# Kernel tuning notes

Hardware: AMD Instinct MI355X
Metric: run time of the kernel (lower is better)

## Reference

```python
import jax, jax.numpy as jnp
import numpy as np

NUM_EMBED = 1024
HEAD_SIZE = 64
B, T = 4, 4096

def setup_inputs() -> dict:
    key = jax.random.key(0)
    kx, kq, kk, kv = jax.random.split(key, 4)
    scale = NUM_EMBED ** -0.5
    return {
        "x": jax.random.normal(kx, (B, T, NUM_EMBED), dtype=jnp.float32),
        "Wq": jax.random.normal(kq, (NUM_EMBED, HEAD_SIZE), dtype=jnp.float32) * scale,
        "Wk": jax.random.normal(kk, (NUM_EMBED, HEAD_SIZE), dtype=jnp.float32) * scale,
        "Wv": jax.random.normal(kv, (NUM_EMBED, HEAD_SIZE), dtype=jnp.float32) * scale,
    }

def reference(x, Wq, Wk, Wv):
    # x: [B,T,C]; Wq/Wk/Wv: [C,H]
    q = jnp.einsum('btc,ch->bth', x, Wq)
    k = jnp.einsum('btc,ch->bth', x, Wk)
    v = jnp.einsum('btc,ch->bth', x, Wv)
    Tq = x.shape[1]
    att = jnp.einsum('bth,bsh->bts', q, k) * (k.shape[-1] ** -0.5)  # [B,T,T]
    causal = jnp.tril(jnp.ones((Tq, Tq), dtype=bool))
    att = jnp.where(causal, att, -jnp.inf)
    att = jax.nn.softmax(att, axis=-1)
    # dropout p=0 (eval mode): identity
    out = jnp.einsum('bts,bsh->bth', att, v)  # [B,T,H]
    return out
```

## Files before the change

### kernel.cpp

```cpp
#include <hip/hip_runtime.h>

#define B_ 4
#define T_ 4096
#define C_ 1024
#define H_ 64

typedef _Float16 half8  __attribute__((ext_vector_type(8)));
typedef _Float16 half4_ __attribute__((ext_vector_type(4)));
typedef float    floatx4 __attribute__((ext_vector_type(4)));

#define MFMA16(a, b, c)  __builtin_amdgcn_mfma_f32_16x16x32_f16(a, b, c, 0, 0, 0)
#define MFMA16K(a, b, c) __builtin_amdgcn_mfma_f32_16x16x16f16(a, b, c, 0, 0, 0)
#define LO4(v) __builtin_shufflevector(v, v, 0, 1, 2, 3)
#define HI4(v) __builtin_shufflevector(v, v, 4, 5, 6, 7)

__global__ __launch_bounds__(256) void pack_w_kn(
    const float* __restrict__ Wq, const float* __restrict__ Wk,
    const float* __restrict__ Wv, _Float16* __restrict__ Wt2)
{
    const int idx  = blockIdx.x * 256 + threadIdx.x;
    const int mt   = idx >> 14;
    const int j    = (idx >> 10) & 15;
    const int f    = (idx >> 9) & 1;
    const int lane = (idx >> 3) & 63;
    const int jj   = idx & 7;
    const int q = lane >> 4, c = lane & 15;
    const int k  = j * 64 + f * 32 + q * 8 + jj;
    const int hp = mt * 16 + c;
    const float* W = (hp < 64) ? Wq : (hp < 128) ? Wk : Wv;
    Wt2[idx] = (_Float16)W[k * H_ + (hp & 63)];
}

__global__ __launch_bounds__(512) void qkv_kn(
    const float* __restrict__ x, const _Float16* __restrict__ Wt2,
    _Float16* __restrict__ Qh, _Float16* __restrict__ Kpk,
    _Float16* __restrict__ Vpk)
{
    __shared__ _Float16 xs[2][32][72];
    const int tid  = threadIdx.x;
    const int lane = tid & 63, w = tid >> 6;
    const int q    = lane >> 4, c = lane & 15;
    const int nt   = w & 1;
    const int mg   = w >> 1;
    const int row0 = blockIdx.x * 32;

    const int srow = tid >> 4, scol = (tid & 15) * 4;
    const float* xg = x + (size_t)(row0 + srow) * C_ + scol;

    floatx4 acc[3];
    #pragma unroll
    for (int i = 0; i < 3; ++i) acc[i] = floatx4{0.f, 0.f, 0.f, 0.f};

    float4 g = *(const float4*)xg;

    for (int j = 0; j < 16; ++j) {
        half4_ hv;
        hv[0] = (_Float16)g.x; hv[1] = (_Float16)g.y;
        hv[2] = (_Float16)g.z; hv[3] = (_Float16)g.w;
        *(half4_*)(&xs[j & 1][srow][scol]) = hv;
        __syncthreads();
        if (j < 15) g = *(const float4*)(xg + (j + 1) * 64);

        const _Float16* xrow = &xs[j & 1][nt * 16 + c][q * 8];
        const half8 b0 = *(const half8*)xrow;
        const half8 b1 = *(const half8*)(xrow + 32);

        half8 a[6];
        #pragma unroll
        for (int i = 0; i < 3; ++i) {
            const size_t fb = ((size_t)((mg * 3 + i) * 16 + j) * 2) * 512 + lane * 8;
            a[i * 2]     = *(const half8*)(Wt2 + fb);
            a[i * 2 + 1] = *(const half8*)(Wt2 + fb + 512);
        }
        #pragma unroll
        for (int i = 0; i < 3; ++i) {
            acc[i] = MFMA16(a[i * 2],     b0, acc[i]);
            acc[i] = MFMA16(a[i * 2 + 1], b1, acc[i]);
        }
    }

    const int row = row0 + nt * 16 + c;
    const int b = row >> 12, t4 = row & (T_ - 1);
    const int kt = t4 >> 6;
    const size_t tbase = ((size_t)b * 64 + kt) * 4096;
    const int mtk = (t4 >> 4) & 3;
    const int kk  = t4 & 63;

    #pragma unroll
    for (int i = 0; i < 3; ++i) {
        const int gi = mg * 3 + i;
        if (gi < 4) {
            half4_ v;
            #pragma unroll
            for (int r = 0; r < 4; ++r) v[r] = (_Float16)acc[i][r];
            *(half4_*)(Qh + (size_t)row * H_ + gi * 16 + q * 4) = v;
        } else if (gi < 8) {
            half4_ v;
            #pragma unroll
            for (int r = 0; r < 4; ++r) v[r] = (_Float16)acc[i][r];
            const int e  = gi - 4;
            const int f  = e >> 1;
            const int qa = (e * 2 + (q >> 1)) & 3;
            *(half4_*)(Kpk + tbase + ((size_t)(mtk * 2 + f) * 64 + qa * 16 + c) * 8
                       + (q & 1) * 4) = v;
        } else {
            const int mtv = gi - 8;
            const int qa2 = (kk >> 2) & 3;
            const int h4  = (kk >> 4) & 1;
            const int f2  = kk >> 5;
            const int i2  = kk & 3;
            #pragma unroll
            for (int r = 0; r < 4; ++r) {
                const int cv = q * 4 + r;
                Vpk[tbase + ((size_t)(mtv * 2 + f2) * 64 + qa2 * 16 + cv) * 8
                    + h4 * 4 + i2] = (_Float16)acc[i][r];
            }
        }
    }
}

__global__ __launch_bounds__(512, 4) void attn_kn(
    const _Float16* __restrict__ Qh, const _Float16* __restrict__ Kpk,
    const _Float16* __restrict__ Vpk, float* __restrict__ out)
{
    __shared__ __align__(16) char smem[36864];
    const int lane = threadIdx.x & 63;
    const int w    = threadIdx.x >> 6;
    const int q    = lane >> 4, c = lane & 15;

    const int bid  = blockIdx.x;
    const int xcd  = bid & 7;
    const int slot = bid >> 3;
    const int b    = xcd >> 1;
    const int t    = 255 - ((slot << 1) | (xcd & 1));
    const int row0 = t * 16;
    const int grow = b * T_ + row0;
    const int nk   = (t >> 2) + 1;

    half8 bq0 = *(const half8*)(Qh + (size_t)(grow + c) * H_ + q * 8);
    half8 bq1 = *(const half8*)(Qh + (size_t)(grow + c) * H_ + 32 + q * 8);
    const _Float16 qs = (_Float16)0.18033688f;
    bq0 *= qs; bq1 *= qs;

    floatx4 o[4];
    #pragma unroll
    for (int i = 0; i < 4; ++i) o[i] = floatx4{0.f, 0.f, 0.f, 0.f};
    float m = -3.0e38f, l = 0.f;

    const _Float16* Kb = Kpk + (size_t)b * 262144;
    const _Float16* Vb = Vpk + (size_t)b * 262144;

    half8 k0[4], k1[4], v0[4], v1[4];
    {
        const _Float16* Kt = Kb + (size_t)w * 4096;
        #pragma unroll
        for (int mt = 0; mt < 4; ++mt) {
            k0[mt] = *(const half8*)(Kt + ((mt * 2)     * 64 + lane) * 8);
            k1[mt] = *(const half8*)(Kt + ((mt * 2 + 1) * 64 + lane) * 8);
        }
    }

    #pragma unroll 1
    for (int kt = w; kt < nk; kt += 8) {
        const int kb = kt * 64;

        floatx4 s[4];
        __builtin_amdgcn_s_setprio(1);
        #pragma unroll
        for (int mt = 0; mt < 4; ++mt) {
            floatx4 z = floatx4{0.f, 0.f, 0.f, 0.f};
            z = MFMA16(k0[mt], bq0, z);
            s[mt] = MFMA16(k1[mt], bq1, z);
        }
        __builtin_amdgcn_s_setprio(0);

        const _Float16* Vt = Vb + (size_t)kt * 4096;
        #pragma unroll
        for (int mt = 0; mt < 4; ++mt) {
            v0[mt] = *(const half8*)(Vt + ((mt * 2)     * 64 + lane) * 8);
            v1[mt] = *(const half8*)(Vt + ((mt * 2 + 1) * 64 + lane) * 8);
        }
        {
            const int ktn = (kt + 8 < nk) ? (kt + 8) : kt;
            const _Float16* Kt = Kb + (size_t)ktn * 4096;
            #pragma unroll
            for (int mt = 0; mt < 4; ++mt) {
                k0[mt] = *(const half8*)(Kt + ((mt * 2)     * 64 + lane) * 8);
                k1[mt] = *(const half8*)(Kt + ((mt * 2 + 1) * 64 + lane) * 8);
            }
        }

        if (kt == nk - 1) {
            #pragma unroll
            for (int mt = 0; mt < 4; ++mt)
                #pragma unroll
                for (int r = 0; r < 4; ++r)
                    if (kb + mt * 16 + q * 4 + r > row0 + c) s[mt][r] = -3.0e38f;
        }

        float mx = s[0][0];
        #pragma unroll
        for (int mt = 0; mt < 4; ++mt)
            #pragma unroll
            for (int r = 0; r < 4; ++r) mx = fmaxf(mx, s[mt][r]);
        mx = fmaxf(mx, __shfl_xor(mx, 16, 64));
        mx = fmaxf(mx, __shfl_xor(mx, 32, 64));
        if (!__all(mx <= m + 8.f)) {
            const float mn    = fmaxf(m, mx);
            const float alpha = exp2f(m - mn);
            l *= alpha;
            #pragma unroll
            for (int mt = 0; mt < 4; ++mt) o[mt] *= alpha;
            m = mn;
        }
        half4_ ph[4];
        float sl = 0.f;
        #pragma unroll
        for (int mt = 0; mt < 4; ++mt)
            #pragma unroll
            for (int r = 0; r < 4; ++r) {
                const float ev = exp2f(s[mt][r] - m);
                sl += ev;
                ph[mt][r] = (_Float16)ev;
            }
        sl += __shfl_xor(sl, 16, 64);
        sl += __shfl_xor(sl, 32, 64);
        l += sl;

        __builtin_amdgcn_s_setprio(1);
        #pragma unroll
        for (int mt = 0; mt < 4; ++mt) {
            o[mt] = MFMA16K(LO4(v0[mt]), ph[0], o[mt]);
            o[mt] = MFMA16K(HI4(v0[mt]), ph[1], o[mt]);
            o[mt] = MFMA16K(LO4(v1[mt]), ph[2], o[mt]);
            o[mt] = MFMA16K(HI4(v1[mt]), ph[3], o[mt]);
        }
        __builtin_amdgcn_s_setprio(0);
    }

    float* Ol = (float*)smem;
    float* Ml = (float*)(smem + 34816);
    float* Ll = (float*)(smem + 35328);
    if (q == 0) Ml[w * 16 + c] = m;
    __syncthreads();
    float M = Ml[c];
    #pragma unroll
    for (int w2 = 1; w2 < 8; ++w2) M = fmaxf(M, Ml[w2 * 16 + c]);
    const float alpha = exp2f(m - M);
    if (q == 0) Ll[w * 16 + c] = l * alpha;
    #pragma unroll
    for (int mt = 0; mt < 4; ++mt)
        #pragma unroll
        for (int r = 0; r < 4; ++r)
            Ol[w * 1088 + (mt * 16 + q * 4 + r) * 17 + c] = o[mt][r] * alpha;
    __syncthreads();

    float L = 0.f;
    #pragma unroll
    for (int w2 = 0; w2 < 8; ++w2) L += Ll[w2 * 16 + c];
    const float inv = 1.f / L;
    const int h0 = w * 8 + q * 2;
    float ox = 0.f, oy = 0.f;
    #pragma unroll
    for (int w2 = 0; w2 < 8; ++w2) {
        ox += Ol[w2 * 1088 + h0 * 17 + c];
        oy += Ol[w2 * 1088 + (h0 + 1) * 17 + c];
    }
    float2 st; st.x = ox * inv; st.y = oy * inv;
    *(float2*)(out + (size_t)(grow + c) * H_ + h0) = st;
}

extern "C" void kernel_launch(void* const* d_in, const int* in_sizes, int n_in,
                              void* d_out, int out_size, void* d_ws, size_t ws_size,
                              hipStream_t stream) {
    const float* x  = (const float*)d_in[0];
    const float* Wq = (const float*)d_in[1];
    const float* Wk = (const float*)d_in[2];
    const float* Wv = (const float*)d_in[3];
    float* out = (float*)d_out;

    _Float16* ws = (_Float16*)d_ws;
    _Float16* Wt2 = ws;
    _Float16* Qh  = ws + 196608;
    _Float16* Kpk = Qh + 1048576;
    _Float16* Vpk = Kpk + 1048576;

    hipLaunchKernelGGL(pack_w_kn, dim3(768), dim3(256), 0, stream, Wq, Wk, Wv, Wt2);
    hipLaunchKernelGGL(qkv_kn, dim3((B_ * T_) / 32), dim3(512), 0, stream,
                       x, Wt2, Qh, Kpk, Vpk);
    hipLaunchKernelGGL(attn_kn, dim3(1024), dim3(512), 0, stream,
                       Qh, Kpk, Vpk, out);
}
```

Measured before the change: 138.0 us.

## Share K/V tiles across warps via LDS and split-K with separate combine kernel

Each attention block now covers 128 query rows, eight waves of 16 rows each, and one of eight interleaved key-tile slices. K/V tiles are staged into double-buffered shared memory so all eight waves reuse the same loaded tile. Partial outputs, row maxima and row sums are written to workspace, and a new combine kernel merges the eight splits and writes the final output. This cuts redundant global K/V traffic per query row but adds block-wide syncs, a large fp32 partial-output round trip through memory, and an extra kernel launch.

```diff
diff --git a/kernel.cpp b/kernel.cpp
--- a/kernel.cpp
+++ b/kernel.cpp
@@ -121,24 +121,30 @@
 
 __global__ __launch_bounds__(512, 4) void attn_kn(
     const _Float16* __restrict__ Qh, const _Float16* __restrict__ Kpk,
-    const _Float16* __restrict__ Vpk, float* __restrict__ out)
+    const _Float16* __restrict__ Vpk, float* __restrict__ Opart,
+    float* __restrict__ Mp, float* __restrict__ Lp)
 {
-    __shared__ __align__(16) char smem[36864];
-    const int lane = threadIdx.x & 63;
-    const int w    = threadIdx.x >> 6;
+    __shared__ __align__(16) _Float16 KVs[2][2][4096];
+    const int tid  = threadIdx.x;
+    const int lane = tid & 63;
+    const int w    = tid >> 6;
     const int q    = lane >> 4, c = lane & 15;
 
     const int bid  = blockIdx.x;
     const int xcd  = bid & 7;
     const int slot = bid >> 3;
     const int b    = xcd >> 1;
-    const int t    = 255 - ((slot << 1) | (xcd & 1));
-    const int row0 = t * 16;
-    const int grow = b * T_ + row0;
-    const int nk   = (t >> 2) + 1;
-
-    half8 bq0 = *(const half8*)(Qh + (size_t)(grow + c) * H_ + q * 8);
-    half8 bq1 = *(const half8*)(Qh + (size_t)(grow + c) * H_ + 32 + q * 8);
+    const int tau  = 31 - (slot >> 2);
+    const int s    = ((slot & 3) << 1) | (xcd & 1);
+    const int row0 = tau * 128;
+    const int wrow0 = row0 + w * 16;
+    const int nk_blk = 2 * tau + 2;
+    const int nk_w   = (wrow0 >> 6) + 1;
+    const int ntb = (s < nk_blk) ? (((nk_blk - 1 - s) >> 3) + 1) : 0;
+
+    const _Float16* qb = Qh + (size_t)(b * T_ + wrow0 + c) * H_;
+    half8 bq0 = *(const half8*)(qb + q * 8);
+    half8 bq1 = *(const half8*)(qb + 32 + q * 8);
     const _Float16 qs = (_Float16)0.18033688f;
     bq0 *= qs; bq1 *= qs;
 
@@ -150,124 +156,181 @@
     const _Float16* Kb = Kpk + (size_t)b * 262144;
     const _Float16* Vb = Vpk + (size_t)b * 262144;
 
-    half8 k0[4], k1[4], v0[4], v1[4];
-    {
-        const _Float16* Kt = Kb + (size_t)w * 4096;
+    if (ntb > 0) {
+        const _Float16* Kt = Kb + (size_t)s * 4096;
+        const _Float16* Vt = Vb + (size_t)s * 4096;
+        *(half8*)(&KVs[0][0][tid * 8]) = *(const half8*)(Kt + tid * 8);
+        *(half8*)(&KVs[0][1][tid * 8]) = *(const half8*)(Vt + tid * 8);
+    }
+    __syncthreads();
+
+    #pragma unroll 1
+    for (int i = 0; i < ntb; ++i) {
+        const int kt = s + 8 * i;
+        const bool more = (i + 1 < ntb);
+        half8 gk, gv;
+        if (more) {
+            const _Float16* Kt = Kb + (size_t)(kt + 8) * 4096;
+            const _Float16* Vt = Vb + (size_t)(kt + 8) * 4096;
+            gk = *(const half8*)(Kt + tid * 8);
+            gv = *(const half8*)(Vt + tid * 8);
+        }
+
+        if (kt < nk_w) {
+            const _Float16* Ks = &KVs[i & 1][0][0];
+            const _Float16* Vs = &KVs[i & 1][1][0];
+
+            floatx4 sS[4];
+            __builtin_amdgcn_s_setprio(1);
+            #pragma unroll
+            for (int mt = 0; mt < 4; ++mt) {
+                const half8 ka = *(const half8*)(Ks + ((mt * 2)     * 64 + lane) * 8);
+                const half8 kb2= *(const half8*)(Ks + ((mt * 2 + 1) * 64 + lane) * 8);
+                floatx4 z = floatx4{0.f, 0.f, 0.f, 0.f};
+                z = MFMA16(ka, bq0, z);
+                sS[mt] = MFMA16(kb2, bq1, z);
+            }
+            __builtin_amdgcn_s_setprio(0);
+
+            if (kt == nk_w - 1) {
+                const int kb0 = kt * 64;
+                #pragma unroll
+                for (int mt = 0; mt < 4; ++mt)
+                    #pragma unroll
+                    for (int r = 0; r < 4; ++r)
+                        if (kb0 + mt * 16 + q * 4 + r > wrow0 + c)
+                            sS[mt][r] = -3.0e38f;
+            }
+
+            float mx = sS[0][0];
+            #pragma unroll
+            for (int mt = 0; mt < 4; ++mt)
+                #pragma unroll
+                for (int r = 0; r < 4; ++r) mx = fmaxf(mx, sS[mt][r]);
+            mx = fmaxf(mx, __shfl_xor(mx, 16, 64));
+            mx = fmaxf(mx, __shfl_xor(mx, 32, 64));
+            if (!__all(mx <= m + 8.f)) {
+                const float mn    = fmaxf(m, mx);
+                const float alpha = exp2f(m - mn);
+                l *= alpha;
+                #pragma unroll
+                for (int mt = 0; mt < 4; ++mt) o[mt] *= alpha;
+                m = mn;
+            }
+            half4_ ph[4];
+            float sl = 0.f;
+            #pragma unroll
+            for (int mt = 0; mt < 4; ++mt)
+                #pragma unroll
+                for (int r = 0; r < 4; ++r) {
+                    const float ev = exp2f(sS[mt][r] - m);
+                    sl += ev;
+                    ph[mt][r] = (_Float16)ev;
+                }
+            sl += __shfl_xor(sl, 16, 64);
+            sl += __shfl_xor(sl, 32, 64);
+            l += sl;
+
+            __builtin_amdgcn_s_setprio(1);
+            #pragma unroll
+            for (int mt = 0; mt < 4; ++mt) {
+                const half8 va = *(const half8*)(Vs + ((mt * 2)     * 64 + lane) * 8);
+                const half8 vb = *(const half8*)(Vs + ((mt * 2 + 1) * 64 + lane) * 8);
+                o[mt] = MFMA16K(LO4(va), ph[0], o[mt]);
+                o[mt] = MFMA16K(HI4(va), ph[1], o[mt]);
+                o[mt] = MFMA16K(LO4(vb), ph[2], o[mt]);
+                o[mt] = MFMA16K(HI4(vb), ph[3], o[mt]);
+            }
+            __builtin_amdgcn_s_setprio(0);
+        }
+
+        __syncthreads();
+        if (more) {
+            *(half8*)(&KVs[(i + 1) & 1][0][tid * 8]) = gk;
+            *(half8*)(&KVs[(i + 1) & 1][1][tid * 8]) = gv;
+            __syncthreads();
+        }
+    }
+
+    float* Ob = Opart + ((size_t)bid * 8 + w) * 1024;
+    #pragma unroll
+    for (int mt = 0; mt < 4; ++mt)
+        *(floatx4*)(Ob + mt * 256 + lane * 4) = o[mt];
+    if (q == 0) {
+        Mp[(size_t)bid * 128 + w * 16 + c] = m;
+        Lp[(size_t)bid * 128 + w * 16 + c] = l;
+    }
+}
+
+__global__ __launch_bounds__(64) void combine_kn(
+    const float* __restrict__ Opart, const float* __restrict__ Mp,
+    const float* __restrict__ Lp, float* __restrict__ out)
+{
+    __shared__ float sO[64][17];
+    const int cb  = blockIdx.x;
+    const int w2  = cb & 7;
+    const int tau = (cb >> 3) & 31;
+    const int b   = cb >> 8;
+    const int lane = threadIdx.x;
+    const int q = lane >> 4, c = lane & 15;
+
+    int items[8];
+    #pragma unroll
+    for (int s = 0; s < 8; ++s) {
+        const int xcd  = b * 2 + (s & 1);
+        const int slot = (31 - tau) * 4 + (s >> 1);
+        items[s] = slot * 8 + xcd;
+    }
+
+    float Mv[8], Lv[8];
+    #pragma unroll
+    for (int s = 0; s < 8; ++s) {
+        Mv[s] = Mp[(size_t)items[s] * 128 + w2 * 16 + c];
+        Lv[s] = Lp[(size_t)items[s] * 128 + w2 * 16 + c];
+    }
+    float M = Mv[0];
+    #pragma unroll
+    for (int s = 1; s < 8; ++s) M = fmaxf(M, Mv[s]);
+    float L = 0.f;
+    float a[8];
+    #pragma unroll
+    for (int s = 0; s < 8; ++s) {
+        a[s] = exp2f(Mv[s] - M);
+        L += Lv[s] * a[s];
+    }
+    const float inv = 1.f / L;
+
+    floatx4 acc[4];
+    #pragma unroll
+    for (int mt = 0; mt < 4; ++mt) acc[mt] = floatx4{0.f, 0.f, 0.f, 0.f};
+    #pragma unroll
+    for (int s = 0; s < 8; ++s) {
+        const float* Ob = Opart + ((size_t)items[s] * 8 + w2) * 1024;
         #pragma unroll
         for (int mt = 0; mt < 4; ++mt) {
-            k0[mt] = *(const half8*)(Kt + ((mt * 2)     * 64 + lane) * 8);
-            k1[mt] = *(const half8*)(Kt + ((mt * 2 + 1) * 64 + lane) * 8);
-        }
-    }
-
-    #pragma unroll 1
-    for (int kt = w; kt < nk; kt += 8) {
-        const int kb = kt * 64;
-
-        floatx4 s[4];
-        __builtin_amdgcn_s_setprio(1);
-        #pragma unroll
-        for (int mt = 0; mt < 4; ++mt) {
-            floatx4 z = floatx4{0.f, 0.f, 0.f, 0.f};
-            z = MFMA16(k0[mt], bq0, z);
-            s[mt] = MFMA16(k1[mt], bq1, z);
-        }
-        __builtin_amdgcn_s_setprio(0);
-
-        const _Float16* Vt = Vb + (size_t)kt * 4096;
-        #pragma unroll
-        for (int mt = 0; mt < 4; ++mt) {
-            v0[mt] = *(const half8*)(Vt + ((mt * 2)     * 64 + lane) * 8);
-            v1[mt] = *(const half8*)(Vt + ((mt * 2 + 1) * 64 + lane) * 8);
-        }
-        {
-            const int ktn = (kt + 8 < nk) ? (kt + 8) : kt;
-            const _Float16* Kt = Kb + (size_t)ktn * 4096;
-            #pragma unroll
-            for (int mt = 0; mt < 4; ++mt) {
-                k0[mt] = *(const half8*)(Kt + ((mt * 2)     * 64 + lane) * 8);
-                k1[mt] = *(const half8*)(Kt + ((mt * 2 + 1) * 64 + lane) * 8);
-            }
-        }
-
-        if (kt == nk - 1) {
-            #pragma unroll
-            for (int mt = 0; mt < 4; ++mt)
-                #pragma unroll
-                for (int r = 0; r < 4; ++r)
-                    if (kb + mt * 16 + q * 4 + r > row0 + c) s[mt][r] = -3.0e38f;
-        }
-
-        float mx = s[0][0];
-        #pragma unroll
-        for (int mt = 0; mt < 4; ++mt)
-            #pragma unroll
-            for (int r = 0; r < 4; ++r) mx = fmaxf(mx, s[mt][r]);
-        mx = fmaxf(mx, __shfl_xor(mx, 16, 64));
-        mx = fmaxf(mx, __shfl_xor(mx, 32, 64));
-        if (!__all(mx <= m + 8.f)) {
-            const float mn    = fmaxf(m, mx);
-            const float alpha = exp2f(m - mn);
-            l *= alpha;
-            #pragma unroll
-            for (int mt = 0; mt < 4; ++mt) o[mt] *= alpha;
-            m = mn;
-        }
-        half4_ ph[4];
-        float sl = 0.f;
-        #pragma unroll
-        for (int mt = 0; mt < 4; ++mt)
-            #pragma unroll
-            for (int r = 0; r < 4; ++r) {
-                const float ev = exp2f(s[mt][r] - m);
-                sl += ev;
-                ph[mt][r] = (_Float16)ev;
-            }
-        sl += __shfl_xor(sl, 16, 64);
-        sl += __shfl_xor(sl, 32, 64);
-        l += sl;
-
-        __builtin_amdgcn_s_setprio(1);
-        #pragma unroll
-        for (int mt = 0; mt < 4; ++mt) {
-            o[mt] = MFMA16K(LO4(v0[mt]), ph[0], o[mt]);
-            o[mt] = MFMA16K(HI4(v0[mt]), ph[1], o[mt]);
-            o[mt] = MFMA16K(LO4(v1[mt]), ph[2], o[mt]);
-            o[mt] = MFMA16K(HI4(v1[mt]), ph[3], o[mt]);
-        }
-        __builtin_amdgcn_s_setprio(0);
-    }
-
-    float* Ol = (float*)smem;
-    float* Ml = (float*)(smem + 34816);
-    float* Ll = (float*)(smem + 35328);
-    if (q == 0) Ml[w * 16 + c] = m;
-    __syncthreads();
-    float M = Ml[c];
-    #pragma unroll
-    for (int w2 = 1; w2 < 8; ++w2) M = fmaxf(M, Ml[w2 * 16 + c]);
-    const float alpha = exp2f(m - M);
-    if (q == 0) Ll[w * 16 + c] = l * alpha;
+            const floatx4 v = *(const floatx4*)(Ob + mt * 256 + lane * 4);
+            acc[mt] += v * a[s];
+        }
+    }
     #pragma unroll
     for (int mt = 0; mt < 4; ++mt)
         #pragma unroll
         for (int r = 0; r < 4; ++r)
-            Ol[w * 1088 + (mt * 16 + q * 4 + r) * 17 + c] = o[mt][r] * alpha;
+            sO[mt * 16 + q * 4 + r][c] = acc[mt][r] * inv;
     __syncthreads();
 
-    float L = 0.f;
-    #pragma unroll
-    for (int w2 = 0; w2 < 8; ++w2) L += Ll[w2 * 16 + c];
-    const float inv = 1.f / L;
-    const int h0 = w * 8 + q * 2;
-    float ox = 0.f, oy = 0.f;
-    #pragma unroll
-    for (int w2 = 0; w2 < 8; ++w2) {
-        ox += Ol[w2 * 1088 + h0 * 17 + c];
-        oy += Ol[w2 * 1088 + (h0 + 1) * 17 + c];
-    }
-    float2 st; st.x = ox * inv; st.y = oy * inv;
-    *(float2*)(out + (size_t)(grow + c) * H_ + h0) = st;
+    const int orow = lane >> 2;
+    const int seg  = lane & 3;
+    float* dst = out + (size_t)(b * T_ + tau * 128 + w2 * 16 + orow) * H_ + seg * 16;
+    #pragma unroll
+    for (int v4 = 0; v4 < 4; ++v4) {
+        float4 vv;
+        vv.x = sO[seg * 16 + v4 * 4 + 0][orow];
+        vv.y = sO[seg * 16 + v4 * 4 + 1][orow];
+        vv.z = sO[seg * 16 + v4 * 4 + 2][orow];
+        vv.w = sO[seg * 16 + v4 * 4 + 3][orow];
+        *(float4*)(dst + v4 * 4) = vv;
+    }
 }
 
 extern "C" void kernel_launch(void* const* d_in, const int* in_sizes, int n_in,
@@ -284,10 +347,15 @@
     _Float16* Qh  = ws + 196608;
     _Float16* Kpk = Qh + 1048576;
     _Float16* Vpk = Kpk + 1048576;
+    float* Opart = (float*)(ws + 3342336);
+    float* Mp    = Opart + 8388608;
+    float* Lp    = Mp + 131072;
 
     hipLaunchKernelGGL(pack_w_kn, dim3(768), dim3(256), 0, stream, Wq, Wk, Wv, Wt2);
     hipLaunchKernelGGL(qkv_kn, dim3((B_ * T_) / 32), dim3(512), 0, stream,
                        x, Wt2, Qh, Kpk, Vpk);
     hipLaunchKernelGGL(attn_kn, dim3(1024), dim3(512), 0, stream,
-                       Qh, Kpk, Vpk, out);
-}
+                       Qh, Kpk, Vpk, Opart, Mp, Lp);
+    hipLaunchKernelGGL(combine_kn, dim3(1024), dim3(64), 0, stream,
+                       Opart, Mp, Lp, out);
+}
```

After: 142.0 us. 2.9% more time.
